# Kernel tuning notes

Measured on AMD Instinct MI355X. Metric: run time of the kernel, lower is better.

Reference implementation:

```python
import jax, jax.numpy as jnp
import numpy as np

# Circuit dimensions (levelized DAG stand-in for the SDD-derived network)
B = 1024          # batch
NUM_VARS = 2048   # propositional variables
LEAVES = 2 * NUM_VARS  # positive + negative literal nodes (smooth circuit)
LEVELS = 12       # internal levels (topological depth)
WIDTH = 4096      # internal nodes per level
FANIN = 4         # children per internal node
TOTAL = LEAVES + LEVELS * WIDTH  # total nodes in execution order


def setup_inputs() -> dict:
    key = jax.random.key(0)
    x = jax.random.uniform(key, (B, NUM_VARS), dtype=jnp.float32)
    rng = np.random.default_rng(0)
    # child_idx[l, i, k]: index (into the global node-output buffer) of the
    # k-th child of node i at level l. DAG constraint: children must be
    # earlier nodes, i.e. index < LEAVES + l * WIDTH.
    child_idx = np.zeros((LEVELS, WIDTH, FANIN), dtype=np.int32)
    for l in range(LEVELS):
        cap = LEAVES + l * WIDTH
        child_idx[l] = rng.integers(0, cap, size=(WIDTH, FANIN), dtype=np.int32)
    # op_type: 0 -> AND node (product of children), 1 -> OR node (sum of children)
    op_type = rng.integers(0, 2, size=(LEVELS, WIDTH)).astype(np.int32)
    return {"x": x,
            "child_idx": jnp.asarray(child_idx),
            "op_type": jnp.asarray(op_type)}


def reference(x, child_idx, op_type):
    """Bottom-up evaluation of the levelized arithmetic circuit.

    x:         [B, NUM_VARS] literal probabilities
    child_idx: [LEVELS, WIDTH, FANIN] int32 child indices (constants)
    op_type:   [LEVELS, WIDTH] int32, 0=AND (prod), 1=OR (sum)
    Returns:   [B] root node output (last node in execution order).
    """
    b = x.shape[0]
    # Leaf (literal/prob node) outputs: [x, 1-x] -> [B, LEAVES]
    leaf = jnp.concatenate([x, 1.0 - x], axis=1)
    buf = jnp.zeros((b, TOTAL), dtype=x.dtype)
    buf = buf.at[:, :LEAVES].set(leaf)
    n_levels = child_idx.shape[0]
    for l in range(n_levels):  # structural loop over circuit depth (small, fixed)
        ch = buf[:, child_idx[l]]                 # gather children: [B, WIDTH, FANIN]
        out = jnp.where(op_type[l] == 0,
                        jnp.prod(ch, axis=-1),    # AND nodes
                        jnp.sum(ch, axis=-1))     # OR nodes
        start = LEAVES + l * WIDTH
        buf = buf.at[:, start:start + WIDTH].set(out)
    return buf[:, -1]  # root output
```

## Files before the change

kernel.cpp:

```cpp
#include <hip/hip_runtime.h>

#define BATCH    1024
#define NUM_VARS 2048
#define LEAVES   (2 * NUM_VARS)
#define LEVELS   12
#define WIDTH    4096
#define TOTAL    (LEAVES + LEVELS * WIDTH)
#define NWORDS   (TOTAL / 32)

#define CAP      2048
#define BSLICE   4
#define NEVB     (BATCH / BSLICE)
#define ETHR     1024

#define ROWS     (NUM_VARS + CAP)
#define LDPAD    8
#define LDSTRIDE (ROWS + LDPAD)
#define SMEM_BYTES (4 * LDSTRIDE * 4 + CAP * 16 + 64)

#define PREF_SPLIT 8
#define NPREF      (LEVELS * PREF_SPLIT)
#define SETUP_GRID (1 + NPREF)


__global__ __launch_bounds__(1024) void setup_kernel(const int4* __restrict__ child4,
                                                     const int*  __restrict__ op_type,
                                                     int4* __restrict__ enc4,
                                                     int*  __restrict__ counts)
{
    const int tid = threadIdx.x;

    if (blockIdx.x >= 1) {
        const int seg   = blockIdx.x - 1;
        const int l     = seg / PREF_SPLIT;
        const int part  = seg % PREF_SPLIT;
        const int cnt   = WIDTH / PREF_SPLIT;
        const int base  = l * WIDTH + part * cnt;
        int acc = 0;
        for (int i = tid; i < cnt; i += 1024) {
            const int4 c = child4[base + i];
            acc ^= c.x ^ c.y ^ c.z ^ c.w ^ op_type[base + i];
        }
        asm volatile("" :: "v"(acc));
        return;
    }

    __shared__ unsigned int flg[NWORDS];
    __shared__ int nid[CAP];
    __shared__ int lvl_cnt[LEVELS], lvl_base[LEVELS];
    __shared__ int total_s;
    const int lane = tid & 63;
    const int wv   = tid >> 6;

    for (int i = tid; i < NWORDS; i += 1024) flg[i] = 0u;
    __syncthreads();
    if (tid == 0) flg[NWORDS - 1] = 0x80000000u;
    __syncthreads();

    for (int l = LEVELS - 1; l >= 0; --l) {
        const int wbase = 128 * (l + 1);
        #pragma unroll
        for (int j = 0; j < 4; ++j) {
            const int k = (tid << 2) | j;
            if ((flg[wbase + (k >> 5)] >> (k & 31)) & 1u) {
                const int4 c = child4[l * WIDTH + k];
                atomicOr(&flg[c.x >> 5], 1u << (c.x & 31));
                atomicOr(&flg[c.y >> 5], 1u << (c.y & 31));
                atomicOr(&flg[c.z >> 5], 1u << (c.z & 31));
                atomicOr(&flg[c.w >> 5], 1u << (c.w & 31));
            }
        }
        __syncthreads();
    }

    if (wv < LEVELS) {
        const unsigned int w0 = flg[128 * (wv + 1) + 2 * lane];
        const unsigned int w1 = flg[128 * (wv + 1) + 2 * lane + 1];
        const int pc = __popc(w0) + __popc(w1);
        int scan = pc;
        for (int d = 1; d < 64; d <<= 1) {
            const int up = __shfl_up(scan, d, 64);
            if (lane >= d) scan += up;
        }
        if (lane == 63) lvl_cnt[wv] = scan;
    }
    __syncthreads();
    if (tid == 0) {
        int s = 0;
        for (int l = 0; l < LEVELS; ++l) { lvl_base[l] = s; s += lvl_cnt[l]; }
        total_s = (s < CAP) ? s : CAP;
        for (int l = 0; l < LEVELS; ++l) counts[l] = lvl_cnt[l];
        counts[LEVELS] = total_s;
    }
    __syncthreads();
    if (wv < LEVELS) {
        const unsigned int w0 = flg[128 * (wv + 1) + 2 * lane];
        const unsigned int w1 = flg[128 * (wv + 1) + 2 * lane + 1];
        const int pc = __popc(w0) + __popc(w1);
        int scan = pc;
        for (int d = 1; d < 64; d <<= 1) {
            const int up = __shfl_up(scan, d, 64);
            if (lane >= d) scan += up;
        }
        int base = lvl_base[wv] + scan - pc;
        const int nd0 = LEAVES + wv * WIDTH + 64 * lane;
        unsigned int w = w0;
        while (w) { const int b = __ffs(w) - 1; w &= w - 1;
                    if (base < CAP) nid[base] = nd0 + b;      base++; }
        w = w1;
        while (w) { const int b = __ffs(w) - 1; w &= w - 1;
                    if (base < CAP) nid[base] = nd0 + 32 + b; base++; }
    }
    __syncthreads();

    const int S = total_s;
    for (int slot = tid; slot < S; slot += 1024) {
        const int nd = nid[slot];
        const int4 c = child4[nd - LEAVES];
        const int  o = op_type[nd - LEAVES];
        int lo0 = 0, lo1 = 0, lo2 = 0, lo3 = 0;
        int hi0 = S, hi1 = S, hi2 = S, hi3 = S;
        #pragma unroll
        for (int it = 0; it < 11; ++it) {
            const int m0 = (lo0 + hi0) >> 1, m1 = (lo1 + hi1) >> 1;
            const int m2 = (lo2 + hi2) >> 1, m3 = (lo3 + hi3) >> 1;
            const int n0 = nid[m0], n1 = nid[m1], n2 = nid[m2], n3 = nid[m3];
            if (lo0 < hi0) { if (n0 < c.x) lo0 = m0 + 1; else hi0 = m0; }
            if (lo1 < hi1) { if (n1 < c.y) lo1 = m1 + 1; else hi1 = m1; }
            if (lo2 < hi2) { if (n2 < c.z) lo2 = m2 + 1; else hi2 = m2; }
            if (lo3 < hi3) { if (n3 < c.w) lo3 = m3 + 1; else hi3 = m3; }
        }
        int4 e;
        e.x = (c.x < NUM_VARS) ? c.x : (c.x < LEAVES) ? ((c.x - NUM_VARS) | 0x4000)
                                                      : (NUM_VARS + lo0);
        e.y = (c.y < NUM_VARS) ? c.y : (c.y < LEAVES) ? ((c.y - NUM_VARS) | 0x4000)
                                                      : (NUM_VARS + lo1);
        e.z = (c.z < NUM_VARS) ? c.z : (c.z < LEAVES) ? ((c.z - NUM_VARS) | 0x4000)
                                                      : (NUM_VARS + lo2);
        e.w = (c.w < NUM_VARS) ? c.w : (c.w < LEAVES) ? ((c.w - NUM_VARS) | 0x4000)
                                                      : (NUM_VARS + lo3);
        e.x |= o << 20;
        enc4[slot] = e;
    }
}

__global__ __launch_bounds__(ETHR) void eval_kernel(const float* __restrict__ x,
                                                    const int4* __restrict__ enc4g,
                                                    const int*  __restrict__ countsg,
                                                    float* __restrict__ out)
{
    extern __shared__ char smem[];
    float* buf      = (float*)smem;
    int4*  enc_s    = (int4*)(smem + 4 * LDSTRIDE * sizeof(float));
    int*   counts_s = (int*)(smem + 4 * LDSTRIDE * sizeof(float) + CAP * sizeof(int4));

    const int tid = threadIdx.x;

    {
        const int c  = tid >> 8;
        const int v0 = tid & 255;
        const float* xr = x + (size_t)(blockIdx.x * BSLICE + c) * NUM_VARS;
        float* br = buf + c * LDSTRIDE;
        #pragma unroll
        for (int k = 0; k < NUM_VARS / 256; ++k)
            br[v0 + k * 256] = xr[v0 + k * 256];
    }
    #pragma unroll
    for (int i = tid; i < CAP; i += ETHR) enc_s[i] = enc4g[i];
    if (tid < LEVELS) counts_s[tid] = countsg[tid];
    __syncthreads();

    const int col = tid & 3;
    const int nl  = tid >> 2;
    float* bc = buf + col * LDSTRIDE;

    int sb = 0;
    for (int l = 0; l < LEVELS; ++l) {
        const int n = counts_s[l];
        for (int i = nl; i < n; i += ETHR / BSLICE) {
            const int4 e = enc_s[sb + i];
            float v0 = bc[e.x & 0x3FFF];
            float v1 = bc[e.y & 0x3FFF];
            float v2 = bc[e.z & 0x3FFF];
            float v3 = bc[e.w & 0x3FFF];
            v0 = (e.x & 0x4000) ? 1.0f - v0 : v0;
            v1 = (e.y & 0x4000) ? 1.0f - v1 : v1;
            v2 = (e.z & 0x4000) ? 1.0f - v2 : v2;
            v3 = (e.w & 0x4000) ? 1.0f - v3 : v3;
            const float p = ((v0 * v1) * v2) * v3;
            const float s = ((v0 + v1) + v2) + v3;
            const float r = (e.x & (1 << 20)) ? s : p;
            bc[NUM_VARS + sb + i] = r;
            if (l == LEVELS - 1 && i == n - 1)
                out[blockIdx.x * BSLICE + col] = r;
        }
        __syncthreads();
        sb += n;
    }
}

extern "C" void kernel_launch(void* const* d_in, const int* in_sizes, int n_in,
                              void* d_out, int out_size, void* d_ws, size_t ws_size,
                              hipStream_t stream)
{
    const float* x       = (const float*)d_in[0];
    const int4*  child4  = (const int4*)d_in[1];
    const int*   op_type = (const int*)d_in[2];
    float*       out     = (float*)d_out;

    char* w = (char*)d_ws;
    int4* enc4   = (int4*)w;  w += (size_t)CAP * sizeof(int4);
    int*  counts = (int*)w;   w += 64;

    static bool lds_opted = false;
    if (!lds_opted) {
        hipFuncSetAttribute((const void*)eval_kernel,
                            hipFuncAttributeMaxDynamicSharedMemorySize, SMEM_BYTES);
        lds_opted = true;
    }

    setup_kernel<<<SETUP_GRID, 1024, 0, stream>>>(child4, op_type, enc4, counts);
    eval_kernel<<<NEVB, ETHR, SMEM_BYTES, stream>>>(x, enc4, counts, out);
}
```

Baseline: 79.32 us.

## Fuse circuit pruning setup into eval kernel, recomputing encoding per block

Merges the single-block setup kernel (backward reachability marking, compaction, child index remapping) into the evaluation kernel, so every block redoes the pruning in LDS instead of reading an encoded table from global memory. This removes a kernel launch and the serial dependency on one setup block, and the leaf x loads are issued as float4 up front so they overlap the setup work. In exchange, all 256 blocks repeat the atomics and binary searches and LDS use grows (flag bitmap and node list added), which may affect occupancy. The LDS row stride changes to 4100.

Measured after the change: 76.38 us. 1.04x faster.

```diff
diff --git a/kernel.cpp b/kernel.cpp
--- a/kernel.cpp
+++ b/kernel.cpp
@@ -14,56 +14,57 @@
 #define ETHR     1024
 
 #define ROWS     (NUM_VARS + CAP)
-#define LDPAD    8
-#define LDSTRIDE (ROWS + LDPAD)
-#define SMEM_BYTES (4 * LDSTRIDE * 4 + CAP * 16 + 64)
+#define LDSTRIDE 4100
 
-#define PREF_SPLIT 8
-#define NPREF      (LEVELS * PREF_SPLIT)
-#define SETUP_GRID (1 + NPREF)
+#define OFF_BUF   0
+#define SZ_BUF    (4 * LDSTRIDE * 4)
+#define OFF_ENC   (OFF_BUF + SZ_BUF)
+#define SZ_ENC    (CAP * 16)
+#define OFF_FLG   (OFF_ENC + SZ_ENC)
+#define SZ_FLG    (NWORDS * 4)
+#define OFF_NID   (OFF_FLG + SZ_FLG)
+#define SZ_NID    ((CAP + 8) * 4)
+#define OFF_MISC  (OFF_NID + SZ_NID)
+#define SMEM_BYTES (OFF_MISC + 128)
 
 
-__global__ __launch_bounds__(1024) void setup_kernel(const int4* __restrict__ child4,
+__global__ __launch_bounds__(ETHR) void fused_kernel(const float* __restrict__ x,
+                                                     const int4* __restrict__ child4,
                                                      const int*  __restrict__ op_type,
-                                                     int4* __restrict__ enc4,
-                                                     int*  __restrict__ counts)
+                                                     float* __restrict__ out)
 {
-    const int tid = threadIdx.x;
+    extern __shared__ char smem[];
+    float*        buf      = (float*)(smem + OFF_BUF);
+    int4*         enc_s    = (int4*)(smem + OFF_ENC);
+    unsigned int* flg      = (unsigned int*)(smem + OFF_FLG);
+    int*          nid      = (int*)(smem + OFF_NID);
+    int*          lvl_cnt  = (int*)(smem + OFF_MISC);
+    int*          lvl_base = lvl_cnt + LEVELS;
+    int*          total_s  = lvl_base + LEVELS;
 
-    if (blockIdx.x >= 1) {
-        const int seg   = blockIdx.x - 1;
-        const int l     = seg / PREF_SPLIT;
-        const int part  = seg % PREF_SPLIT;
-        const int cnt   = WIDTH / PREF_SPLIT;
-        const int base  = l * WIDTH + part * cnt;
-        int acc = 0;
-        for (int i = tid; i < cnt; i += 1024) {
-            const int4 c = child4[base + i];
-            acc ^= c.x ^ c.y ^ c.z ^ c.w ^ op_type[base + i];
-        }
-        asm volatile("" :: "v"(acc));
-        return;
-    }
-
-    __shared__ unsigned int flg[NWORDS];
-    __shared__ int nid[CAP];
-    __shared__ int lvl_cnt[LEVELS], lvl_base[LEVELS];
-    __shared__ int total_s;
+    const int tid  = threadIdx.x;
     const int lane = tid & 63;
     const int wv   = tid >> 6;
 
-    for (int i = tid; i < NWORDS; i += 1024) flg[i] = 0u;
-    __syncthreads();
-    if (tid == 0) flg[NWORDS - 1] = 0x80000000u;
+    const int pc_ = tid >> 8;
+    const int pq  = tid & 255;
+    const float4* xr4 =
+        (const float4*)(x + (size_t)(blockIdx.x * BSLICE + pc_) * NUM_VARS);
+    const float4 lf0 = xr4[pq];
+    const float4 lf1 = xr4[pq + 256];
+
+    for (int i = tid; i < NWORDS; i += ETHR)
+        flg[i] = (i == NWORDS - 1) ? 0x80000000u : 0u;
     __syncthreads();
 
     for (int l = LEVELS - 1; l >= 0; --l) {
         const int wbase = 128 * (l + 1);
+        const unsigned int fw = flg[wbase + (tid >> 3)];
+        const int sh = (tid & 7) * 4;
         #pragma unroll
         for (int j = 0; j < 4; ++j) {
-            const int k = (tid << 2) | j;
-            if ((flg[wbase + (k >> 5)] >> (k & 31)) & 1u) {
-                const int4 c = child4[l * WIDTH + k];
+            if ((fw >> (sh + j)) & 1u) {
+                const int4 c = child4[l * WIDTH + ((tid << 2) | j)];
                 atomicOr(&flg[c.x >> 5], 1u << (c.x & 31));
                 atomicOr(&flg[c.y >> 5], 1u << (c.y & 31));
                 atomicOr(&flg[c.z >> 5], 1u << (c.z & 31));
@@ -88,11 +89,10 @@
     if (tid == 0) {
         int s = 0;
         for (int l = 0; l < LEVELS; ++l) { lvl_base[l] = s; s += lvl_cnt[l]; }
-        total_s = (s < CAP) ? s : CAP;
-        for (int l = 0; l < LEVELS; ++l) counts[l] = lvl_cnt[l];
-        counts[LEVELS] = total_s;
+        *total_s = (s < CAP) ? s : CAP;
     }
     __syncthreads();
+
     if (wv < LEVELS) {
         const unsigned int w0 = flg[128 * (wv + 1) + 2 * lane];
         const unsigned int w1 = flg[128 * (wv + 1) + 2 * lane + 1];
@@ -113,8 +113,8 @@
     }
     __syncthreads();
 
-    const int S = total_s;
-    for (int slot = tid; slot < S; slot += 1024) {
+    const int S = *total_s;
+    for (int slot = tid; slot < S; slot += ETHR) {
         const int nd = nid[slot];
         const int4 c = child4[nd - LEAVES];
         const int  o = op_type[nd - LEAVES];
@@ -140,43 +140,23 @@
         e.w = (c.w < NUM_VARS) ? c.w : (c.w < LEAVES) ? ((c.w - NUM_VARS) | 0x4000)
                                                       : (NUM_VARS + lo3);
         e.x |= o << 20;
-        enc4[slot] = e;
+        enc_s[slot] = e;
     }
-}
-
-__global__ __launch_bounds__(ETHR) void eval_kernel(const float* __restrict__ x,
-                                                    const int4* __restrict__ enc4g,
-                                                    const int*  __restrict__ countsg,
-                                                    float* __restrict__ out)
-{
-    extern __shared__ char smem[];
-    float* buf      = (float*)smem;
-    int4*  enc_s    = (int4*)(smem + 4 * LDSTRIDE * sizeof(float));
-    int*   counts_s = (int*)(smem + 4 * LDSTRIDE * sizeof(float) + CAP * sizeof(int4));
-
-    const int tid = threadIdx.x;
 
     {
-        const int c  = tid >> 8;
-        const int v0 = tid & 255;
-        const float* xr = x + (size_t)(blockIdx.x * BSLICE + c) * NUM_VARS;
-        float* br = buf + c * LDSTRIDE;
-        #pragma unroll
-        for (int k = 0; k < NUM_VARS / 256; ++k)
-            br[v0 + k * 256] = xr[v0 + k * 256];
+        float* br = buf + pc_ * LDSTRIDE;
+        ((float4*)br)[pq]       = lf0;
+        ((float4*)br)[pq + 256] = lf1;
     }
-    #pragma unroll
-    for (int i = tid; i < CAP; i += ETHR) enc_s[i] = enc4g[i];
-    if (tid < LEVELS) counts_s[tid] = countsg[tid];
     __syncthreads();
 
     const int col = tid & 3;
     const int nl  = tid >> 2;
     float* bc = buf + col * LDSTRIDE;
 
-    int sb = 0;
     for (int l = 0; l < LEVELS; ++l) {
-        const int n = counts_s[l];
+        const int n  = lvl_cnt[l];
+        const int sb = lvl_base[l];
         for (int i = nl; i < n; i += ETHR / BSLICE) {
             const int4 e = enc_s[sb + i];
             float v0 = bc[e.x & 0x3FFF];
@@ -195,7 +175,6 @@
                 out[blockIdx.x * BSLICE + col] = r;
         }
         __syncthreads();
-        sb += n;
     }
 }
 
@@ -207,18 +186,14 @@
     const int4*  child4  = (const int4*)d_in[1];
     const int*   op_type = (const int*)d_in[2];
     float*       out     = (float*)d_out;
-
-    char* w = (char*)d_ws;
-    int4* enc4   = (int4*)w;  w += (size_t)CAP * sizeof(int4);
-    int*  counts = (int*)w;   w += 64;
+    (void)d_ws; (void)ws_size;
 
     static bool lds_opted = false;
     if (!lds_opted) {
-        hipFuncSetAttribute((const void*)eval_kernel,
+        hipFuncSetAttribute((const void*)fused_kernel,
                             hipFuncAttributeMaxDynamicSharedMemorySize, SMEM_BYTES);
         lds_opted = true;
     }
 
-    setup_kernel<<<SETUP_GRID, 1024, 0, stream>>>(child4, op_type, enc4, counts);
-    eval_kernel<<<NEVB, ETHR, SMEM_BYTES, stream>>>(x, enc4, counts, out);
+    fused_kernel<<<NEVB, ETHR, SMEM_BYTES, stream>>>(x, child4, op_type, out);
 }
```
